# Kernel optimization log

Measured on AMD Instinct MI355X. Metric: run time of the kernel, lower is better.

## Reference

```python
import jax, jax.numpy as jnp
import numpy as np

HIDDEN = 1152
NUM_HEADS = 16
HEAD_DIM = HIDDEN // NUM_HEADS  # 72
SEQ = 4096


def rotate_half(x):
    x1 = x[..., : x.shape[-1] // 2]
    x2 = x[..., x.shape[-1] // 2 :]
    return jnp.concatenate((-x2, x1), axis=-1)


def setup_inputs() -> dict:
    key = jax.random.key(0)
    ks = jax.random.split(key, 8)
    hidden_states = jax.random.normal(ks[0], (SEQ, HIDDEN), dtype=jnp.float32)
    cu_seqlens = jnp.sort(jax.random.randint(ks[1], (3,), 0, SEQ)).astype(jnp.int32)
    # rotary embeddings: realistic cos/sin tables
    pos = jnp.arange(SEQ, dtype=jnp.float32)[:, None]
    inv_freq = 1.0 / (10000.0 ** (jnp.arange(0, HEAD_DIM, 2, dtype=jnp.float32) / HEAD_DIM))
    freqs = pos * inv_freq[None, :]  # (SEQ, HEAD_DIM//2)
    emb = jnp.concatenate([freqs, freqs], axis=-1)  # (SEQ, HEAD_DIM)
    cos = jnp.cos(emb)
    sin = jnp.sin(emb)
    std = 0.02
    Wqkv = jax.random.normal(ks[2], (HIDDEN, 3 * HIDDEN), dtype=jnp.float32) * std
    bqkv = jnp.zeros((3 * HIDDEN,), dtype=jnp.float32)
    Wproj = jax.random.normal(ks[3], (HIDDEN, HIDDEN), dtype=jnp.float32) * std
    bproj = jnp.zeros((HIDDEN,), dtype=jnp.float32)
    return {
        "hidden_states": hidden_states,
        "cu_seqlens": cu_seqlens,
        "cos": cos,
        "sin": sin,
        "Wqkv": Wqkv,
        "bqkv": bqkv,
        "Wproj": Wproj,
        "bproj": bproj,
    }


def reference(hidden_states, cu_seqlens, cos, sin, Wqkv, bqkv, Wproj, bproj):
    seq_len = hidden_states.shape[0]
    scale = HEAD_DIM ** -0.5
    qkv = hidden_states @ Wqkv + bqkv  # (S, 3*H)
    qkv = qkv.reshape(seq_len, 3, NUM_HEADS, HEAD_DIM).transpose(1, 0, 2, 3)
    q, k, v = qkv[0], qkv[1], qkv[2]  # each (S, nH, hd)
    # inline RoPE in fp32
    orig_dtype = q.dtype
    qf = q.astype(jnp.float32)
    kf = k.astype(jnp.float32)
    c = cos[:, None, :].astype(jnp.float32)
    s = sin[:, None, :].astype(jnp.float32)
    q = (qf * c + rotate_half(qf) * s).astype(orig_dtype)
    k = (kf * c + rotate_half(kf) * s).astype(orig_dtype)
    # (nH, S, hd)
    q = q.transpose(1, 0, 2)
    k = k.transpose(1, 0, 2)
    v = v.transpose(1, 0, 2)
    attn = jnp.einsum('hqd,hkd->hqk', q, k) * scale
    attn = jax.nn.softmax(attn, axis=-1)
    out = jnp.einsum('hqk,hkd->hqd', attn, v)  # (nH, S, hd)
    out = out.transpose(1, 0, 2).reshape(seq_len, HIDDEN)
    return out @ Wproj + bproj
```

## Files before the change

kernel.cpp:

```cpp
#include <hip/hip_runtime.h>
#include <hip/hip_bf16.h>
#include <stdint.h>

#define SEQ 4096
#define HID 1152
#define NH  16
#define HD  72
#define N3  3456
#define DQ  80
#define QBLK 256
#define TILE_ELEMS 14336

typedef __bf16 bf16;
typedef __bf16 bf16x8 __attribute__((ext_vector_type(8)));
typedef float  f32x4  __attribute__((ext_vector_type(4)));
typedef float  f32x16 __attribute__((ext_vector_type(16)));
typedef uint32_t u32x4 __attribute__((ext_vector_type(4)));

#define EXP2F(x) __builtin_amdgcn_exp2f(x)
#define PLSWAP(a, b) asm("v_permlane32_swap_b32 %0, %1" : "+v"(a), "+v"(b))

__device__ __forceinline__ void gload_lds16(const void* g, void* l) {
    __builtin_amdgcn_global_load_lds(
        (__attribute__((address_space(1))) void*)(void*)g,
        (__attribute__((address_space(3))) void*)l, 16, 0, 0);
}
__device__ __forceinline__ uint16_t bfbits(float x) {
    return __builtin_bit_cast(uint16_t, (bf16)x);
}

__device__ __forceinline__ int xcd_swz(int orig, int nwg) {
    return (orig & 7) * (nwg >> 3) + (orig >> 3);
}

__global__ __launch_bounds__(256)
void prep(const float* __restrict__ hidden, const float* __restrict__ Wqkv,
          const float* __restrict__ Wproj, bf16* __restrict__ hid_b,
          bf16* __restrict__ WqkvT, bf16* __restrict__ WprojT)
{
    __shared__ float tl[32][33];
    int b = blockIdx.x, tid = threadIdx.x;
    if (b < 2304) {
        int i = b * 256 + tid;
        const float4* p = (const float4*)hidden + (size_t)i * 2;
        float4 a = p[0], c = p[1];
        bf16x8 o;
        o[0]=(bf16)a.x; o[1]=(bf16)a.y; o[2]=(bf16)a.z; o[3]=(bf16)a.w;
        o[4]=(bf16)c.x; o[5]=(bf16)c.y; o[6]=(bf16)c.z; o[7]=(bf16)c.w;
        ((bf16x8*)hid_b)[i] = o;
        return;
    }
    const float* in; bf16* out; int R, C, c0, r0;
    if (b < 6192) {
        int bb = b - 2304;
        in = Wqkv; out = WqkvT; R = HID; C = N3;
        c0 = (bb % 108) * 32; r0 = (bb / 108) * 32;
    } else {
        int bb = b - 6192;
        in = Wproj; out = WprojT; R = HID; C = HID;
        c0 = (bb % 36) * 32; r0 = (bb / 36) * 32;
    }
    int tx = tid & 31, ty = tid >> 5;
#pragma unroll
    for (int i = 0; i < 4; ++i)
        tl[ty + 8*i][tx] = in[(size_t)(r0 + ty + 8*i) * C + c0 + tx];
    __syncthreads();
#pragma unroll
    for (int i = 0; i < 4; ++i)
        out[(size_t)(c0 + ty + 8*i) * R + r0 + tx] = (bf16)tl[tx][ty + 8*i];
}

template<int OUT_F32>
__global__ __launch_bounds__(256)
void gemm_bt(const bf16* __restrict__ A, const bf16* __restrict__ BT,
             const float* __restrict__ bias, void* __restrict__ out,
             int M, int N, int K)
{
    __shared__ __align__(16) bf16 As[128 * 64];
    __shared__ __align__(16) bf16 Bs[128 * 64];
    int tid = threadIdx.x;
    int lane = tid & 63, w = tid >> 6;
    int wm = w & 1, wn = w >> 1;
    int nwg  = gridDim.x * gridDim.y;
    int wgid = xcd_swz(blockIdx.y * gridDim.x + blockIdx.x, nwg);
    int m0 = (wgid % gridDim.x) * 128, n0 = (wgid / gridDim.x) * 128;
    int lq = lane & 15, lk = lane >> 4;

    int kx0 = ((lk ^ (lq & 7)) << 4);
    int kx1 = (((4 + lk) ^ (lq & 7)) << 4);

    f32x4 acc[4][4] = {};

    for (int k0 = 0; k0 < K; k0 += 64) {
        __syncthreads();
#pragma unroll
        for (int j = 0; j < 4; ++j) {
            int c = j * 256 + tid;
            int row = c >> 3, kc = c & 7;
            int koff = k0 + ((kc ^ (row & 7)) << 3);
            gload_lds16(A  + (size_t)(m0 + row) * K + koff, (char*)As + c * 16);
            gload_lds16(BT + (size_t)(n0 + row) * K + koff, (char*)Bs + c * 16);
        }
        __syncthreads();
#pragma unroll
        for (int ks = 0; ks < 2; ++ks) {
            int kx = ks ? kx1 : kx0;
            bf16x8 af[4], bfr[4];
#pragma unroll
            for (int m = 0; m < 4; ++m)
                af[m] = *(const bf16x8*)((char*)As + (wm * 64 + m * 16 + lq) * 128 + kx);
#pragma unroll
            for (int n = 0; n < 4; ++n)
                bfr[n] = *(const bf16x8*)((char*)Bs + (wn * 64 + n * 16 + lq) * 128 + kx);
#pragma unroll
            for (int m = 0; m < 4; ++m)
#pragma unroll
                for (int n = 0; n < 4; ++n)
                    acc[m][n] = __builtin_amdgcn_mfma_f32_16x16x32_bf16(af[m], bfr[n], acc[m][n], 0, 0, 0);
        }
    }

    int rb = m0 + wm * 64, cb = n0 + wn * 64;
#pragma unroll
    for (int m = 0; m < 4; ++m) {
#pragma unroll
        for (int n = 0; n < 4; ++n) {
            int col = cb + n * 16 + lq;
            float b = bias[col];
#pragma unroll
            for (int r = 0; r < 4; ++r) {
                int row = rb + m * 16 + lk * 4 + r;
                float v = acc[m][n][r] + b;
                if (OUT_F32) ((float*)out)[(size_t)row * N + col] = v;
                else         ((bf16*)out)[(size_t)row * N + col] = (bf16)v;
            }
        }
    }
}

__global__ __launch_bounds__(256)
void pack(const bf16* __restrict__ qkv, const float* __restrict__ cs,
          const float* __restrict__ sn, bf16* __restrict__ Qp,
          bf16* __restrict__ KVp)
{
    __shared__ __align__(16) bf16 tl[64][80];
    int b = blockIdx.x, tid = threadIdx.x;
    if (b < 32768) {
        int idx = b * 256 + tid;
        int dd = idx & 127;
        int s  = (idx >> 7) & (SEQ - 1);
        int h  = idx >> 19;
        float qv = 0.f, kv = 0.f;
        if (dd < HD) {
            const bf16* row = qkv + (size_t)s * N3 + h * HD;
            float c  = cs[s * HD + dd], si = sn[s * HD + dd];
            int   dp = (dd < 36) ? dd + 36 : dd - 36;
            float sg = (dd < 36) ? -1.f : 1.f;
            float qa = (float)row[dd],       qb = (float)row[dp];
            float ka = (float)row[HID + dd], kb = (float)row[HID + dp];
            qv = (qa * c + sg * qb * si) * (0.11785113019775793f * 1.4426950408889634f);
            kv =  ka * c + sg * kb * si;
        }
        int t = s >> 6, key = s & 63;
        int chunk = key * 16 + ((dd >> 3) ^ (key & 15));
        KVp[((size_t)(h * 64 + t)) * TILE_ELEMS + chunk * 8 + (dd & 7)] = (bf16)kv;
        if (dd < DQ) Qp[((size_t)h * SEQ + s) * DQ + dd] = (bf16)qv;
        return;
    }
    int bb = b - 32768;
    int t = bb & 63, h = bb >> 6, s0 = t * 64;
    for (int i = tid; i < 64 * 9; i += 256) {
        int key = i / 9, c8 = (i % 9) * 8;
        *(bf16x8*)&tl[key][c8] =
            *(const bf16x8*)&qkv[(size_t)(s0 + key) * N3 + 2 * HID + h * HD + c8];
    }
    __syncthreads();
    bf16* dst = KVp + ((size_t)(h * 64 + t)) * TILE_ELEMS + 8192;
    for (int vcid = tid; vcid < 768; vcid += 256) {
        int d = vcid >> 3, cpos = vcid & 7;
        int kb8 = (cpos ^ (d & 7)) << 3;
        bf16x8 v;
#pragma unroll
        for (int j = 0; j < 8; ++j)
            v[j] = (d < HD) ? tl[kb8 + j][d] : ((d == HD) ? (bf16)1.f : (bf16)0.f);
        *(bf16x8*)&dst[vcid * 8] = v;
    }
}

__global__ __launch_bounds__(512, 2)
void attn_fwd11(const bf16* __restrict__ Qp, const bf16* __restrict__ KVp,
                bf16* __restrict__ Oout)
{
    __shared__ __align__(16) char smem[86016];

    const int o = blockIdx.x;
    const int x = o & 7, s = o >> 3;
    const int h  = x * 2 + (s >> 4);
    const int q0 = (s & 15) * QBLK;
    const int tid = threadIdx.x, lane = tid & 63, w = tid >> 6;
    const int ql = lane & 31, hi = lane >> 5;
    const int q  = q0 + w * 32 + ql;

    bf16x8 qf[5];
    const bf16* qbase = Qp + ((size_t)h * SEQ + q) * DQ + hi * 8;
#pragma unroll
    for (int ks = 0; ks < 5; ++ks) qf[ks] = *(const bf16x8*)(qbase + ks * 16);

    int aK[5], aV[4];
#pragma unroll
    for (int ks = 0; ks < 5; ++ks)
        aK[ks] = ql * 256 + (((ks * 2 + hi) ^ (ql & 15)) * 16);
#pragma unroll
    for (int u = 0; u < 4; ++u)
        aV[u] = 16384 + ql * 128 + (((u * 2 + hi) ^ (ql & 7)) * 16);

    f32x16 o_[3] = {};

    const bf16* kvbase = KVp + (size_t)h * (64 * TILE_ELEMS) + (size_t)tid * 8;

#define STAGE(T, DB) do {                                                      \
        const bf16* s_ = kvbase + (size_t)(T) * TILE_ELEMS;                    \
        char* d_ = smem + (DB) + tid * 16;                                     \
        _Pragma("unroll")                                                      \
        for (int j_ = 0; j_ < 3; ++j_)                                         \
            gload_lds16(s_ + j_ * 4096, d_ + j_ * 8192);                       \
        if (tid < 256) gload_lds16(s_ + 12288, d_ + 24576);                    \
    } while (0)

    auto qk = [&](const char* bK, f32x16& sa, f32x16& sb) {
        __builtin_amdgcn_s_setprio(1);
#pragma unroll
        for (int ks = 0; ks < 5; ++ks) {
            bf16x8 kf = *(const bf16x8*)(bK + aK[ks]);
            sa = __builtin_amdgcn_mfma_f32_32x32x16_bf16(kf, qf[ks], sa, 0, 0, 0);
        }
#pragma unroll
        for (int ks = 0; ks < 5; ++ks) {
            bf16x8 kf = *(const bf16x8*)(bK + 8192 + aK[ks]);
            sb = __builtin_amdgcn_mfma_f32_32x32x16_bf16(kf, qf[ks], sb, 0, 0, 0);
        }
        __builtin_amdgcn_s_setprio(0);
    };

    auto expv = [&](const f32x16& sa, const f32x16& sb, const char* bV) {
        uint32_t wd[16];
#pragma unroll
        for (int i = 0; i < 8; ++i) {
            wd[i]   = (uint32_t)bfbits(EXP2F(sa[2*i])) | ((uint32_t)bfbits(EXP2F(sa[2*i+1])) << 16);
            wd[8+i] = (uint32_t)bfbits(EXP2F(sb[2*i])) | ((uint32_t)bfbits(EXP2F(sb[2*i+1])) << 16);
        }
        PLSWAP(wd[0], wd[2]);   PLSWAP(wd[1], wd[3]);
        PLSWAP(wd[4], wd[6]);   PLSWAP(wd[5], wd[7]);
        PLSWAP(wd[8], wd[10]);  PLSWAP(wd[9], wd[11]);
        PLSWAP(wd[12], wd[14]); PLSWAP(wd[13], wd[15]);
        u32x4 u0 = {wd[0],wd[1],wd[2],wd[3]},   u1 = {wd[4],wd[5],wd[6],wd[7]};
        u32x4 u2 = {wd[8],wd[9],wd[10],wd[11]}, u3 = {wd[12],wd[13],wd[14],wd[15]};
        bf16x8 pb[4] = { __builtin_bit_cast(bf16x8, u0), __builtin_bit_cast(bf16x8, u1),
                         __builtin_bit_cast(bf16x8, u2), __builtin_bit_cast(bf16x8, u3) };
        __builtin_amdgcn_s_setprio(1);
#pragma unroll
        for (int db = 0; db < 3; ++db)
#pragma unroll
            for (int u = 0; u < 4; ++u) {
                bf16x8 vf = *(const bf16x8*)(bV + db * 4096 + aV[u]);
                o_[db] = __builtin_amdgcn_mfma_f32_32x32x16_bf16(vf, pb[u], o_[db], 0, 0, 0);
            }
        __builtin_amdgcn_s_setprio(0);
    };

    f32x16 pa = {}, pb_ = {};

    STAGE(0, 0);
    asm volatile("s_waitcnt vmcnt(0)" ::: "memory");
    __builtin_amdgcn_s_barrier();
    STAGE(1, 28672);
    qk(smem, pa, pb_);
    asm volatile("s_waitcnt vmcnt(0)" ::: "memory");
    __builtin_amdgcn_s_barrier();

#define BODY(T, KB, VB, SB) do {                                               \
        if ((T) < 63) STAGE((T) + 1, SB);                                      \
        f32x16 ca = {}, cb = {};                                               \
        qk(smem + (KB), ca, cb);                                               \
        expv(pa, pb_, smem + (VB));                                            \
        pa = ca; pb_ = cb;                                                     \
        __builtin_amdgcn_sched_barrier(0);                                     \
        asm volatile("s_waitcnt vmcnt(0)" ::: "memory");                       \
        __builtin_amdgcn_s_barrier();                                          \
    } while (0)

    for (int t = 1; t < 64; t += 3) {
        BODY(t,     28672, 0,     57344);
        BODY(t + 1, 57344, 28672, 0);
        BODY(t + 2, 0,     57344, 28672);
    }
    expv(pa, pb_, smem);
#undef BODY
#undef STAGE

    __syncthreads();
    bf16* Os = (bf16*)smem;
    {
        float lv  = o_[2][4];
        float lo_ = __shfl_xor(lv, 32);
        float invl = 1.0f / (hi ? lo_ : lv);
        int qloc = w * 32 + ql;
#pragma unroll
        for (int db = 0; db < 3; ++db)
#pragma unroll
            for (int r = 0; r < 16; ++r) {
                int dloc = (r & 3) + 8 * (r >> 2) + 4 * hi;
                int d = db * 32 + dloc;
                if (d < HD) Os[qloc * 82 + d] = (bf16)(o_[db][r] * invl);
            }
    }
    __syncthreads();
    for (int i = tid; i < QBLK * 36; i += 512) {
        int row = i / 36, c = i % 36;
        uint32_t val = *(const uint32_t*)((const char*)Os + row * 164 + c * 4);
        *(uint32_t*)((char*)Oout + (size_t)(q0 + row) * 2304 + h * 144 + c * 4) = val;
    }
}

extern "C" void kernel_launch(void* const* d_in, const int* in_sizes, int n_in,
                              void* d_out, int out_size, void* d_ws, size_t ws_size,
                              hipStream_t stream)
{
    const float* hidden = (const float*)d_in[0];
    const float* cosT  = (const float*)d_in[2];
    const float* sinT  = (const float*)d_in[3];
    const float* Wqkv  = (const float*)d_in[4];
    const float* bqkv  = (const float*)d_in[5];
    const float* Wproj = (const float*)d_in[6];
    const float* bproj = (const float*)d_in[7];

    char* ws = (char*)d_ws;
    size_t off = 0;
    auto alloc = [&](size_t bytes) {
        char* p = ws + off;
        off += (bytes + 255) & ~(size_t)255;
        return p;
    };
    bf16* hid_b  = (bf16*)alloc((size_t)SEQ * HID * 2);
    bf16* WqkvT  = (bf16*)alloc((size_t)N3  * HID * 2);
    bf16* WprojT = (bf16*)alloc((size_t)HID * HID * 2);
    bf16* qkv_b  = (bf16*)alloc((size_t)SEQ * N3  * 2);
    bf16* Qp     = (bf16*)alloc((size_t)NH * SEQ * DQ * 2);
    bf16* KVp    = (bf16*)alloc((size_t)NH * 64 * TILE_ELEMS * 2);
    bf16* attno  = hid_b;

    prep<<<7488, 256, 0, stream>>>(hidden, Wqkv, Wproj, hid_b, WqkvT, WprojT);
    gemm_bt<0><<<dim3(SEQ / 128, N3 / 128), 256, 0, stream>>>(hid_b, WqkvT, bqkv, qkv_b,
                                                              SEQ, N3, HID);
    pack<<<33792, 256, 0, stream>>>(qkv_b, cosT, sinT, Qp, KVp);
    attn_fwd11<<<dim3(SEQ / QBLK * NH), 512, 0, stream>>>(Qp, KVp, attno);
    gemm_bt<1><<<dim3(SEQ / 128, HID / 128), 256, 0, stream>>>(attno, WprojT, bproj, d_out,
                                                               SEQ, HID, HID);
}
```

Measured before the change: 205.1 us.

## Fuse RoPE and Q/KV packing into QKV GEMM epilogue with head-aligned tiles

Replaces the generic QKV GEMM and the separate pack kernel with a dedicated GEMM that uses 128x144 tiles covering two whole heads. In the epilogue the tile is staged in LDS, then RoPE, the Q scale and the swizzled Q/K/V layouts are applied and written straight to the attention input buffers. Padding and ones-column initialisation moves into extra blocks of the prep kernel. This removes the intermediate qkv buffer round-trip and one launch, at the cost of a less tuned GEMM tile and a scalar, possibly poorly coalesced epilogue store.

```diff
diff --git a/kernel.cpp b/kernel.cpp
--- a/kernel.cpp
+++ b/kernel.cpp
@@ -19,6 +19,7 @@
 
 #define EXP2F(x) __builtin_amdgcn_exp2f(x)
 #define PLSWAP(a, b) asm("v_permlane32_swap_b32 %0, %1" : "+v"(a), "+v"(b))
+#define QSCALE (0.11785113019775793f * 1.4426950408889634f)
 
 __device__ __forceinline__ void gload_lds16(const void* g, void* l) {
     __builtin_amdgcn_global_load_lds(
@@ -36,7 +37,8 @@
 __global__ __launch_bounds__(256)
 void prep(const float* __restrict__ hidden, const float* __restrict__ Wqkv,
           const float* __restrict__ Wproj, bf16* __restrict__ hid_b,
-          bf16* __restrict__ WqkvT, bf16* __restrict__ WprojT)
+          bf16* __restrict__ WqkvT, bf16* __restrict__ WprojT,
+          bf16* __restrict__ Qp, bf16* __restrict__ KVp)
 {
     __shared__ float tl[32][33];
     int b = blockIdx.x, tid = threadIdx.x;
@@ -50,6 +52,30 @@
         ((bf16x8*)hid_b)[i] = o;
         return;
     }
+    if (b >= 7488) {
+        bf16x8 zero = {};
+        if (b < 7744) {
+            int idx = (b - 7488) * 256 + tid;
+            int h = idx >> 12, s = idx & 4095;
+            *(bf16x8*)&Qp[((size_t)(h * 4096 + s)) * DQ + 72] = zero;
+        } else if (b < 9536) {
+            int flat = (b - 7744) * 256 + tid;
+            int j7 = flat % 7, rest = flat / 7;
+            int key = rest & 63, t = (rest >> 6) & 63, h = rest >> 12;
+            int pos = key * 16 + ((9 + j7) ^ (key & 15));
+            *(bf16x8*)&KVp[((size_t)(h * 64 + t)) * TILE_ELEMS + pos * 8] = zero;
+        } else {
+            int flat = (b - 9536) * 256 + tid;
+            int j = flat & 7, d = 72 + ((flat >> 3) % 24);
+            int t = (flat / 192) & 63, h = flat / 12288;
+            bf16x8 v = zero;
+            if (d == 72)
+#pragma unroll
+                for (int e = 0; e < 8; ++e) v[e] = (bf16)1.f;
+            *(bf16x8*)&KVp[((size_t)(h * 64 + t)) * TILE_ELEMS + 8192 + d * 64 + j * 8] = v;
+        }
+        return;
+    }
     const float* in; bf16* out; int R, C, c0, r0;
     if (b < 6192) {
         int bb = b - 2304;
@@ -68,6 +94,103 @@
 #pragma unroll
     for (int i = 0; i < 4; ++i)
         out[(size_t)(c0 + ty + 8*i) * R + r0 + tx] = (bf16)tl[tx][ty + 8*i];
+}
+
+__global__ __launch_bounds__(256)
+void gemm_qkv(const bf16* __restrict__ A, const bf16* __restrict__ BT,
+              const float* __restrict__ bias, const float* __restrict__ cs,
+              const float* __restrict__ sn, bf16* __restrict__ Qp,
+              bf16* __restrict__ KVp)
+{
+    __shared__ __align__(16) char smem[36864];
+    bf16* Ep = (bf16*)smem;
+    int tid = threadIdx.x;
+    int lane = tid & 63, w = tid >> 6;
+    int wgid = xcd_swz(blockIdx.x, gridDim.x);
+    int m0 = (wgid & 31) * 128;
+    int ntile = wgid >> 5;
+    int n0 = ntile * 144;
+    int lq = lane & 15, lk = lane >> 4;
+
+    int kx0 = ((lk ^ (lq & 7)) << 4);
+    int kx1 = (((4 + lk) ^ (lq & 7)) << 4);
+
+    f32x4 acc[2][9] = {};
+
+    for (int k0 = 0; k0 < HID; k0 += 64) {
+        __syncthreads();
+#pragma unroll
+        for (int j = 0; j < 9; ++j) {
+            int c = j * 256 + tid;
+            if (j < 4) {
+                int row = c >> 3, kc = c & 7;
+                gload_lds16(A + (size_t)(m0 + row) * HID + k0 + ((kc ^ (row & 7)) << 3),
+                            smem + c * 16);
+            } else if (j < 8 || tid < 128) {
+                int c2 = c - 1024;
+                int row = c2 >> 3, kc = c2 & 7;
+                gload_lds16(BT + (size_t)(n0 + row) * HID + k0 + ((kc ^ (row & 7)) << 3),
+                            smem + 16384 + c2 * 16);
+            }
+        }
+        __syncthreads();
+#pragma unroll
+        for (int ks = 0; ks < 2; ++ks) {
+            int kx = ks ? kx1 : kx0;
+            bf16x8 af[2], bfr[9];
+#pragma unroll
+            for (int m = 0; m < 2; ++m)
+                af[m] = *(const bf16x8*)(smem + (w * 32 + m * 16 + lq) * 128 + kx);
+#pragma unroll
+            for (int n = 0; n < 9; ++n)
+                bfr[n] = *(const bf16x8*)(smem + 16384 + (n * 16 + lq) * 128 + kx);
+#pragma unroll
+            for (int m = 0; m < 2; ++m)
+#pragma unroll
+                for (int n = 0; n < 9; ++n)
+                    acc[m][n] = __builtin_amdgcn_mfma_f32_16x16x32_bf16(af[m], bfr[n], acc[m][n], 0, 0, 0);
+        }
+    }
+
+    __syncthreads();
+#pragma unroll
+    for (int m = 0; m < 2; ++m)
+#pragma unroll
+        for (int n = 0; n < 9; ++n) {
+            float bv = bias[n0 + n * 16 + lq];
+#pragma unroll
+            for (int r = 0; r < 4; ++r)
+                Ep[(w * 32 + m * 16 + lk * 4 + r) * 144 + n * 16 + lq] =
+                    (bf16)(acc[m][n][r] + bv);
+        }
+    __syncthreads();
+
+    int sec = n0 / HID;
+    int h0 = (n0 - sec * HID) / HD;
+    for (int i = tid; i < 128 * 144; i += 256) {
+        int row = i / 144, c = i % 144;
+        int s = m0 + row;
+        int hh = h0 + (c >= 72);
+        int d = c - ((c >= 72) ? 72 : 0);
+        float v = (float)Ep[row * 144 + c];
+        int key = s & 63, t = s >> 6;
+        if (sec == 2) {
+            size_t base = ((size_t)(hh * 64 + t)) * TILE_ELEMS + 8192;
+            KVp[base + d * 64 + (((key >> 3) ^ (d & 7)) << 3) + (key & 7)] = (bf16)v;
+        } else {
+            int dp  = (d < 36) ? d + 36 : d - 36;
+            float sg = (d < 36) ? -1.f : 1.f;
+            float v2 = (float)Ep[row * 144 + (c - d + dp)];
+            float cv = cs[s * HD + d], sv = sn[s * HD + d];
+            float ov = v * cv + sg * v2 * sv;
+            if (sec == 0) {
+                Qp[((size_t)hh * SEQ + s) * DQ + d] = (bf16)(ov * QSCALE);
+            } else {
+                size_t base = ((size_t)(hh * 64 + t)) * TILE_ELEMS;
+                KVp[base + (key * 16 + ((d >> 3) ^ (key & 15))) * 8 + (d & 7)] = (bf16)ov;
+            }
+        }
+    }
 }
 
 template<int OUT_F32>
@@ -138,55 +261,6 @@
     }
 }
 
-__global__ __launch_bounds__(256)
-void pack(const bf16* __restrict__ qkv, const float* __restrict__ cs,
-          const float* __restrict__ sn, bf16* __restrict__ Qp,
-          bf16* __restrict__ KVp)
-{
-    __shared__ __align__(16) bf16 tl[64][80];
-    int b = blockIdx.x, tid = threadIdx.x;
-    if (b < 32768) {
-        int idx = b * 256 + tid;
-        int dd = idx & 127;
-        int s  = (idx >> 7) & (SEQ - 1);
-        int h  = idx >> 19;
-        float qv = 0.f, kv = 0.f;
-        if (dd < HD) {
-            const bf16* row = qkv + (size_t)s * N3 + h * HD;
-            float c  = cs[s * HD + dd], si = sn[s * HD + dd];
-            int   dp = (dd < 36) ? dd + 36 : dd - 36;
-            float sg = (dd < 36) ? -1.f : 1.f;
-            float qa = (float)row[dd],       qb = (float)row[dp];
-            float ka = (float)row[HID + dd], kb = (float)row[HID + dp];
-            qv = (qa * c + sg * qb * si) * (0.11785113019775793f * 1.4426950408889634f);
-            kv =  ka * c + sg * kb * si;
-        }
-        int t = s >> 6, key = s & 63;
-        int chunk = key * 16 + ((dd >> 3) ^ (key & 15));
-        KVp[((size_t)(h * 64 + t)) * TILE_ELEMS + chunk * 8 + (dd & 7)] = (bf16)kv;
-        if (dd < DQ) Qp[((size_t)h * SEQ + s) * DQ + dd] = (bf16)qv;
-        return;
-    }
-    int bb = b - 32768;
-    int t = bb & 63, h = bb >> 6, s0 = t * 64;
-    for (int i = tid; i < 64 * 9; i += 256) {
-        int key = i / 9, c8 = (i % 9) * 8;
-        *(bf16x8*)&tl[key][c8] =
-            *(const bf16x8*)&qkv[(size_t)(s0 + key) * N3 + 2 * HID + h * HD + c8];
-    }
-    __syncthreads();
-    bf16* dst = KVp + ((size_t)(h * 64 + t)) * TILE_ELEMS + 8192;
-    for (int vcid = tid; vcid < 768; vcid += 256) {
-        int d = vcid >> 3, cpos = vcid & 7;
-        int kb8 = (cpos ^ (d & 7)) << 3;
-        bf16x8 v;
-#pragma unroll
-        for (int j = 0; j < 8; ++j)
-            v[j] = (d < HD) ? tl[kb8 + j][d] : ((d == HD) ? (bf16)1.f : (bf16)0.f);
-        *(bf16x8*)&dst[vcid * 8] = v;
-    }
-}
-
 __global__ __launch_bounds__(512, 2)
 void attn_fwd11(const bf16* __restrict__ Qp, const bf16* __restrict__ KVp,
                 bf16* __restrict__ Oout)
@@ -344,15 +418,12 @@
     bf16* hid_b  = (bf16*)alloc((size_t)SEQ * HID * 2);
     bf16* WqkvT  = (bf16*)alloc((size_t)N3  * HID * 2);
     bf16* WprojT = (bf16*)alloc((size_t)HID * HID * 2);
-    bf16* qkv_b  = (bf16*)alloc((size_t)SEQ * N3  * 2);
     bf16* Qp     = (bf16*)alloc((size_t)NH * SEQ * DQ * 2);
     bf16* KVp    = (bf16*)alloc((size_t)NH * 64 * TILE_ELEMS * 2);
     bf16* attno  = hid_b;
 
-    prep<<<7488, 256, 0, stream>>>(hidden, Wqkv, Wproj, hid_b, WqkvT, WprojT);
-    gemm_bt<0><<<dim3(SEQ / 128, N3 / 128), 256, 0, stream>>>(hid_b, WqkvT, bqkv, qkv_b,
-                                                              SEQ, N3, HID);
-    pack<<<33792, 256, 0, stream>>>(qkv_b, cosT, sinT, Qp, KVp);
+    prep<<<10304, 256, 0, stream>>>(hidden, Wqkv, Wproj, hid_b, WqkvT, WprojT, Qp, KVp);
+    gemm_qkv<<<768, 256, 0, stream>>>(hid_b, WqkvT, bqkv, cosT, sinT, Qp, KVp);
     attn_fwd11<<<dim3(SEQ / QBLK * NH), 512, 0, stream>>>(Qp, KVp, attno);
     gemm_bt<1><<<dim3(SEQ / 128, HID / 128), 256, 0, stream>>>(attno, WprojT, bproj, d_out,
                                                                SEQ, HID, HID);
```

New measurement: 240.7 us. +17.4%, slower.
